# Performance work log

Measured on AMD Instinct MI355X. Metric: run time of the kernel, lower is better.

The kernel has to match this reference:

```python
import jax, jax.numpy as jnp
import numpy as np

B, P, D_IN = 128, 4096, 4   # frames, points/frame, xyz+time
NG = 16                      # number of trajectory groups
H1, H2, H3 = 64, 128, 512    # PointNet shared-MLP widths


def _init_mlp(key, dims):
    ks = jax.random.split(key, len(dims) - 1)
    params = []
    for k, (di, do) in zip(ks, zip(dims[:-1], dims[1:])):
        W = jax.random.normal(k, (di, do), dtype=jnp.float32) * (1.0 / np.sqrt(di))
        b = jnp.zeros((do,), dtype=jnp.float32)
        params.append((W, b))
    return params


def setup_inputs() -> dict:
    key = jax.random.key(0)
    k_pc, k_t, k_idx, k_g, k_l = jax.random.split(key, 5)
    pc = jax.random.normal(k_pc, (B, 3, P), dtype=jnp.float32)
    traj_time_batch = jax.random.uniform(k_t, (B, 1), dtype=jnp.float32)
    traj_inbatch_index = jnp.sort(jax.random.randint(k_idx, (B,), 0, NG)).astype(jnp.int32)
    (Wg1, bg1), (Wg2, bg2), (Wg3, bg3) = _init_mlp(k_g, [D_IN, H1, H2, H3])
    (Wl1, bl1), (Wl2, bl2), (Wl3, bl3) = _init_mlp(k_l, [D_IN, H1, H2, H3])
    return dict(pc=pc, traj_time_batch=traj_time_batch, traj_inbatch_index=traj_inbatch_index,
                Wg1=Wg1, bg1=bg1, Wg2=Wg2, bg2=bg2, Wg3=Wg3, bg3=bg3,
                Wl1=Wl1, bl1=bl1, Wl2=Wl2, bl2=bl2, Wl3=Wl3, bl3=bl3)


def _mlp(x, layers):
    # pointwise shared MLP: x [..., P, d_in] -> [..., P, d_out]
    for W, b in layers:
        x = jax.nn.relu(x @ W + b)
    return x


def reference(pc, traj_time_batch, traj_inbatch_index,
              Wg1, bg1, Wg2, bg2, Wg3, bg3,
              Wl1, bl1, Wl2, bl2, Wl3, bl3):
    b, _, p = pc.shape
    # append time channel: [B,3,P] + [B,1,P] -> [B,4,P]
    t = jnp.broadcast_to(traj_time_batch[..., None], (b, 1, p))
    feat = jnp.concatenate([pc, t], axis=1)
    x = jnp.swapaxes(feat, 1, 2)  # [B,P,4] points-last layout for pointwise MLP

    # global branch: shared MLP on every point, then max over all points of each trajectory group
    hg = _mlp(x, [(Wg1, bg1), (Wg2, bg2), (Wg3, bg3)])           # [B,P,H3]
    seg = jnp.repeat(traj_inbatch_index, p)                       # [B*P]
    gmax = jax.ops.segment_max(hg.reshape(b * p, -1), seg, num_segments=NG)  # [NG,H3]
    global_feat = gmax[traj_inbatch_index]                        # [B,H3] broadcast back per frame

    # local branch: per-frame PointNet encode (shared MLP + max over points)
    hl = _mlp(x, [(Wl1, bl1), (Wl2, bl2), (Wl3, bl3)])            # [B,P,H3]
    local_feat = hl.max(axis=1)                                   # [B,H3]

    z = jnp.concatenate([global_feat, local_feat], axis=1)        # [B,2*H3]
    input_features_vis = pc                                       # original pc (last dim == 4096, no slice)
    return (z, input_features_vis)
```

## Files before the change

kernel.cpp:

```cpp
#include <hip/hip_runtime.h>
#include <hip/hip_bf16.h>

#define NB   128
#define NP   4096
#define NGRP 16
#define C3   512

typedef __bf16 bf16x8 __attribute__((ext_vector_type(8)));
typedef __bf16 bf16x4 __attribute__((ext_vector_type(4)));
typedef float  f32x4  __attribute__((ext_vector_type(4)));

#define WS_W1F_G 0
#define WS_W1F_L 4096
#define WS_W2F_G 8192
#define WS_W2F_L 24576
#define WS_W3F_G 40960
#define WS_W3F_L 172032
#define WS_GMAX  303104

__global__ __launch_bounds__(256) void prep_kernel(
    const float* __restrict__ Wg1, const float* __restrict__ Wg2, const float* __restrict__ Wg3,
    const float* __restrict__ Wl1, const float* __restrict__ Wl2, const float* __restrict__ Wl3,
    char* __restrict__ ws) {
    const int t = blockIdx.x, tid = threadIdx.x;
    if (t == 36) {
        float* gmax = (float*)(ws + WS_GMAX);
        #pragma unroll
        for (int k = 0; k < 32; ++k) gmax[k * 256 + tid] = 0.0f;
        int c = tid >> 6, lane = tid & 63;
        int ch = c * 16 + (lane & 15);
        int kb = (lane >> 4) * 8;
        bf16x8 pg, pl;
        #pragma unroll
        for (int j = 0; j < 8; ++j) {
            int k = kb + j;
            pg[j] = (k < 4) ? (__bf16)Wg1[k * 64 + ch] : (__bf16)0.0f;
            pl[j] = (k < 4) ? (__bf16)Wl1[k * 64 + ch] : (__bf16)0.0f;
        }
        *(bf16x8*)((__bf16*)(ws + WS_W1F_G) + c * 512 + lane * 8) = pg;
        *(bf16x8*)((__bf16*)(ws + WS_W1F_L) + c * 512 + lane * 8) = pl;
        return;
    }
    __shared__ float tile[64][65];
    const float* src; __bf16* dst; int cBase, mMul, srcStride;
    if (t < 32) {
        int branch = t >> 4, rem = t & 15;
        int tk = rem >> 3, tc = rem & 7;
        src = (branch ? Wl3 : Wg3) + (size_t)(tk * 64) * 512 + tc * 64;
        dst = (__bf16*)(ws + (branch ? WS_W3F_L : WS_W3F_G));
        cBase = tc * 16 + tk * 2; mMul = 4; srcStride = 512;
    } else {
        int u = t - 32; int branch = u >> 1, tc = u & 1;
        src = (branch ? Wl2 : Wg2) + tc * 64;
        dst = (__bf16*)(ws + (branch ? WS_W2F_L : WS_W2F_G));
        cBase = tc * 8; mMul = 2; srcStride = 128;
    }
    {
        int r0 = tid >> 6, cl = tid & 63;
        #pragma unroll
        for (int p = 0; p < 16; ++p)
            tile[p * 4 + r0][cl] = src[(size_t)(p * 4 + r0) * srcStride + cl];
    }
    __syncthreads();
    int lane = tid & 63, l15 = lane & 15, q = lane >> 4;
    #pragma unroll
    for (int cc = 0; cc < 2; ++cc) {
        int pair = (tid >> 6) * 2 + cc;
        int mi = pair >> 1, ks = pair & 1;
        bf16x8 pk;
        #pragma unroll
        for (int j = 0; j < 8; ++j) pk[j] = (__bf16)tile[ks * 32 + q * 8 + j][mi * 16 + l15];
        *(bf16x8*)(dst + (cBase + mi * mMul + ks) * 512 + lane * 8) = pk;
    }
}

__global__ __launch_bounds__(512, 2) void main_kernel(
    const float* __restrict__ pc, const float* __restrict__ tt, const int* __restrict__ idx,
    const float* __restrict__ bg1, const float* __restrict__ bg2, const float* __restrict__ bg3,
    const float* __restrict__ bl1, const float* __restrict__ bl2, const float* __restrict__ bl3,
    float* __restrict__ out, char* __restrict__ ws) {
    __shared__ __align__(16) char smem[82688];
    __bf16* h2f = (__bf16*)smem;
    __bf16* h1f = (__bf16*)(smem + 65536);
    float*  b1s = (float*)(smem + 81920);
    float*  b2s = (float*)(smem + 82176);

    const int tid = threadIdx.x, lane = tid & 63, wave = tid >> 6;
    const int quad = lane >> 4, l15 = lane & 15;
    const int branch = blockIdx.y, frame = blockIdx.x;
    const int half = wave >> 2;
    const int slice = wave & 3;

    if (branch == 0) {
        const f32x4* ps = (const f32x4*)(pc + (size_t)frame * 3 * NP);
        f32x4* pd = (f32x4*)(out + NB * 2 * C3 + (size_t)frame * 3 * NP);
        #pragma unroll
        for (int j = 0; j < 6; ++j) pd[j * 512 + tid] = ps[j * 512 + tid];
    }

    const __bf16* w1g = (const __bf16*)(ws + (branch ? WS_W1F_L : WS_W1F_G));
    const __bf16* w2g = (const __bf16*)(ws + (branch ? WS_W2F_L : WS_W2F_G));
    const __bf16* w3g = (const __bf16*)(ws + (branch ? WS_W3F_L : WS_W3F_G));
    const float* b1 = branch ? bl1 : bg1;
    const float* b2 = branch ? bl2 : bg2;
    const float* b3 = branch ? bl3 : bg3;

    if (tid < 64)  b1s[tid] = b1[tid];
    if (tid < 128) b2s[tid] = b2[tid];

    bf16x8 a1[4];
    #pragma unroll
    for (int mi = 0; mi < 4; ++mi) a1[mi] = *(const bf16x8*)(w1g + mi * 512 + lane * 8);
    bf16x8 a2[2][2];
    #pragma unroll
    for (int mi = 0; mi < 2; ++mi)
        #pragma unroll
        for (int ks = 0; ks < 2; ++ks)
            a2[mi][ks] = *(const bf16x8*)(w2g + ((slice * 2 + mi) * 2 + ks) * 512 + lane * 8);
    bf16x8 aw[8][4];
    #pragma unroll
    for (int mi = 0; mi < 8; ++mi)
        #pragma unroll
        for (int ks = 0; ks < 4; ++ks)
            aw[mi][ks] = *(const bf16x8*)(w3g + ((slice * 8 + mi) * 4 + ks) * 512 + lane * 8);

    const float tval = tt[frame];
    const f32x4 zf = {0.0f, 0.0f, 0.0f, 0.0f};
    f32x4 runmax[8];
    #pragma unroll
    for (int mi = 0; mi < 8; ++mi) runmax[mi] = (f32x4){-1e30f, -1e30f, -1e30f, -1e30f};

    const float* pcx = pc + (size_t)frame * 3 * NP;
    const int pw = wave * 16 + l15;

    auto do_l1 = [&](float xx, float xy, float xz) {
        bf16x8 xb;
        #pragma unroll
        for (int j = 0; j < 8; ++j) xb[j] = (__bf16)0.0f;
        if (quad == 0) { xb[0] = (__bf16)xx; xb[1] = (__bf16)xy; xb[2] = (__bf16)xz; xb[3] = (__bf16)tval; }
        #pragma unroll
        for (int mi = 0; mi < 4; ++mi) {
            f32x4 c = __builtin_amdgcn_mfma_f32_16x16x32_bf16(a1[mi], xb, zf, 0, 0, 0);
            f32x4 bv = *(const f32x4*)(b1s + mi * 16 + quad * 4);
            bf16x4 pk;
            #pragma unroll
            for (int r = 0; r < 4; ++r) pk[r] = (__bf16)fmaxf(c[r] + bv[r], 0.0f);
            const int kq = (mi & 1) * 2 + (quad >> 1);
            *(bf16x4*)(h1f + (wave * 2 + (mi >> 1)) * 512 + kq * 128 + l15 * 8 + (quad & 1) * 4) = pk;
        }
    };
    auto do_l2 = [&](__bf16* hbn) {
        #pragma unroll
        for (int ni = 0; ni < 4; ++ni) {
            const int p16 = half * 4 + ni;
            bf16x8 q0 = *(const bf16x8*)(h1f + (p16 * 2 + 0) * 512 + lane * 8);
            bf16x8 q1 = *(const bf16x8*)(h1f + (p16 * 2 + 1) * 512 + lane * 8);
            #pragma unroll
            for (int mi = 0; mi < 2; ++mi) {
                f32x4 c = __builtin_amdgcn_mfma_f32_16x16x32_bf16(a2[mi][0], q0, zf, 0, 0, 0);
                c = __builtin_amdgcn_mfma_f32_16x16x32_bf16(a2[mi][1], q1, c, 0, 0, 0);
                f32x4 bv = *(const f32x4*)(b2s + slice * 32 + mi * 16 + quad * 4);
                bf16x4 pk;
                #pragma unroll
                for (int r = 0; r < 4; ++r) pk[r] = (__bf16)fmaxf(c[r] + bv[r], 0.0f);
                const int kq = mi * 2 + (quad >> 1);
                *(bf16x4*)(hbn + (p16 * 4 + slice) * 512 + kq * 128 + l15 * 8 + (quad & 1) * 4) = pk;
            }
        }
    };
    auto p2_pair = [&](const __bf16* hb, int p16base) {
        bf16x8 bhA[4], bhB[4];
        #pragma unroll
        for (int ks = 0; ks < 4; ++ks)
            bhA[ks] = *(const bf16x8*)(hb + (p16base * 4 + ks) * 512 + lane * 8);
        #pragma unroll
        for (int ks = 0; ks < 4; ++ks)
            bhB[ks] = *(const bf16x8*)(hb + ((p16base + 1) * 4 + ks) * 512 + lane * 8);
        #pragma unroll
        for (int u = 0; u < 2; ++u) {
            const bf16x8* cur = u ? bhB : bhA;
            #pragma unroll
            for (int mi = 0; mi < 8; ++mi) {
                f32x4 acc = __builtin_amdgcn_mfma_f32_16x16x32_bf16(aw[mi][0], cur[0], zf, 0, 0, 0);
                acc = __builtin_amdgcn_mfma_f32_16x16x32_bf16(aw[mi][1], cur[1], acc, 0, 0, 0);
                acc = __builtin_amdgcn_mfma_f32_16x16x32_bf16(aw[mi][2], cur[2], acc, 0, 0, 0);
                acc = __builtin_amdgcn_mfma_f32_16x16x32_bf16(aw[mi][3], cur[3], acc, 0, 0, 0);
                #pragma unroll
                for (int r = 0; r < 4; ++r) runmax[mi][r] = fmaxf(runmax[mi][r], acc[r]);
            }
        }
    };

    __syncthreads();

    {
        float xx = pcx[pw], xy = pcx[NP + pw], xz = pcx[2 * NP + pw];
        do_l1(xx, xy, xz);
        __syncthreads();
        do_l2(h2f);
    }

    for (int m = 0; m < 32; ++m) {
        __syncthreads();
        const __bf16* hb = h2f + (m & 1) * 16384;
        __bf16* hbn = h2f + ((m + 1) & 1) * 16384;
        const bool more = (m < 31);
        float nx = 0.f, ny = 0.f, nz = 0.f;
        if (more) {
            const int p = (m + 1) * 128 + pw;
            nx = pcx[p]; ny = pcx[NP + p]; nz = pcx[2 * NP + p];
        }
        p2_pair(hb, half * 4 + 0);
        if (more) do_l1(nx, ny, nz);
        __syncthreads();
        p2_pair(hb, half * 4 + 2);
        if (more) do_l2(hbn);
    }

    __syncthreads();
    float* fscr = (float*)h1f;
    #pragma unroll
    for (int mi = 0; mi < 8; ++mi) {
        f32x4 v = runmax[mi];
        #pragma unroll
        for (int d = 1; d < 16; d <<= 1) {
            #pragma unroll
            for (int r = 0; r < 4; ++r) v[r] = fmaxf(v[r], __shfl_xor(v[r], d));
        }
        if (l15 == 0) {
            #pragma unroll
            for (int r = 0; r < 4; ++r)
                fscr[half * 512 + slice * 128 + mi * 16 + quad * 4 + r] = v[r];
        }
    }
    __syncthreads();
    {
        const int g = idx[frame];
        float* gmax = (float*)(ws + WS_GMAX);
        float v = fmaxf(fscr[tid], fscr[512 + tid]);
        v = fmaxf(v + b3[tid], 0.0f);
        if (branch == 0)
            atomicMax((unsigned*)(gmax + g * C3 + tid), __float_as_uint(v));
        else
            out[(size_t)frame * (2 * C3) + C3 + tid] = v;
    }
}

__global__ void gather_kernel(const int* __restrict__ idx, const char* __restrict__ ws,
                              float* __restrict__ out) {
    int i = blockIdx.x * blockDim.x + threadIdx.x;
    int b = i >> 9, ch = i & 511;
    const float* gmax = (const float*)(ws + WS_GMAX);
    out[b * (2 * C3) + ch] = gmax[idx[b] * C3 + ch];
}

extern "C" void kernel_launch(void* const* d_in, const int* in_sizes, int n_in,
                              void* d_out, int out_size, void* d_ws, size_t ws_size,
                              hipStream_t stream) {
    const float* pc  = (const float*)d_in[0];
    const float* tt  = (const float*)d_in[1];
    const int*   idx = (const int*)d_in[2];
    const float* Wg1 = (const float*)d_in[3];  const float* bg1 = (const float*)d_in[4];
    const float* Wg2 = (const float*)d_in[5];  const float* bg2 = (const float*)d_in[6];
    const float* Wg3 = (const float*)d_in[7];  const float* bg3 = (const float*)d_in[8];
    const float* Wl1 = (const float*)d_in[9];  const float* bl1 = (const float*)d_in[10];
    const float* Wl2 = (const float*)d_in[11]; const float* bl2 = (const float*)d_in[12];
    const float* Wl3 = (const float*)d_in[13]; const float* bl3 = (const float*)d_in[14];
    float* out = (float*)d_out;
    char*  ws  = (char*)d_ws;

    prep_kernel<<<37, 256, 0, stream>>>(Wg1, Wg2, Wg3, Wl1, Wl2, Wl3, ws);
    main_kernel<<<dim3(128, 2), 512, 0, stream>>>(pc, tt, idx, bg1, bg2, bg3,
                                                  bl1, bl2, bl3, out, ws);
    gather_kernel<<<256, 256, 0, stream>>>(idx, ws, out);
}
```

Baseline: 242.8 us.

## Split each frame's points across four blocks and merge maxima with atomics

Each frame's 4096 points are now spread over four blocks of 1024 points, so the main kernel launches 1024 blocks instead of 256. Per-block shared memory and registers are halved, and the launch bound now requests four blocks per CU. Partial maxima are merged with atomicMax directly into the output and the group workspace, so the prep kernel zeroes the local-feature outputs first. This is meant to improve occupancy and load balance on a GPU with many CUs. The cost is more atomics and reloading the per-wave weight fragments in four times as many blocks.

```diff
diff --git a/kernel.cpp b/kernel.cpp
--- a/kernel.cpp
+++ b/kernel.cpp
@@ -21,8 +21,13 @@
 __global__ __launch_bounds__(256) void prep_kernel(
     const float* __restrict__ Wg1, const float* __restrict__ Wg2, const float* __restrict__ Wg3,
     const float* __restrict__ Wl1, const float* __restrict__ Wl2, const float* __restrict__ Wl3,
-    char* __restrict__ ws) {
+    float* __restrict__ out, char* __restrict__ ws) {
     const int t = blockIdx.x, tid = threadIdx.x;
+    if (t >= 37) {
+        #pragma unroll
+        for (int j = 0; j < 8; ++j) out[(t - 37) * 2048 + j * 256 + tid] = 0.0f;
+        return;
+    }
     if (t == 36) {
         float* gmax = (float*)(ws + WS_GMAX);
         #pragma unroll
@@ -74,28 +79,31 @@
     }
 }
 
-__global__ __launch_bounds__(512, 2) void main_kernel(
+__global__ __launch_bounds__(512, 4) void main_kernel(
     const float* __restrict__ pc, const float* __restrict__ tt, const int* __restrict__ idx,
     const float* __restrict__ bg1, const float* __restrict__ bg2, const float* __restrict__ bg3,
     const float* __restrict__ bl1, const float* __restrict__ bl2, const float* __restrict__ bl3,
     float* __restrict__ out, char* __restrict__ ws) {
-    __shared__ __align__(16) char smem[82688];
+    __shared__ __align__(16) char smem[41728];
     __bf16* h2f = (__bf16*)smem;
-    __bf16* h1f = (__bf16*)(smem + 65536);
-    float*  b1s = (float*)(smem + 81920);
-    float*  b2s = (float*)(smem + 82176);
+    __bf16* h1f = (__bf16*)(smem + 32768);
+    float*  b1s = (float*)(smem + 40960);
+    float*  b2s = (float*)(smem + 41216);
 
     const int tid = threadIdx.x, lane = tid & 63, wave = tid >> 6;
     const int quad = lane >> 4, l15 = lane & 15;
-    const int branch = blockIdx.y, frame = blockIdx.x;
-    const int half = wave >> 2;
-    const int slice = wave & 3;
+    const int branch = blockIdx.y;
+    const int frame = blockIdx.x >> 2, p0 = (blockIdx.x & 3) * 1024;
+
+    const float* pcx = pc + (size_t)frame * 3 * NP;
 
     if (branch == 0) {
-        const f32x4* ps = (const f32x4*)(pc + (size_t)frame * 3 * NP);
-        f32x4* pd = (f32x4*)(out + NB * 2 * C3 + (size_t)frame * 3 * NP);
-        #pragma unroll
-        for (int j = 0; j < 6; ++j) pd[j * 512 + tid] = ps[j * 512 + tid];
+        f32x4* pd = (f32x4*)(out + NB * 2 * C3 + (size_t)frame * 3 * NP + p0);
+        const f32x4* ps = (const f32x4*)(pcx + p0);
+        for (int i = tid; i < 768; i += 512) {
+            int r = i >> 8, col = i & 255;
+            pd[r * (NP / 4) + col] = ps[r * (NP / 4) + col];
+        }
     }
 
     const __bf16* w1g = (const __bf16*)(ws + (branch ? WS_W1F_L : WS_W1F_G));
@@ -111,27 +119,27 @@
     bf16x8 a1[4];
     #pragma unroll
     for (int mi = 0; mi < 4; ++mi) a1[mi] = *(const bf16x8*)(w1g + mi * 512 + lane * 8);
-    bf16x8 a2[2][2];
-    #pragma unroll
-    for (int mi = 0; mi < 2; ++mi)
-        #pragma unroll
-        for (int ks = 0; ks < 2; ++ks)
-            a2[mi][ks] = *(const bf16x8*)(w2g + ((slice * 2 + mi) * 2 + ks) * 512 + lane * 8);
-    bf16x8 aw[8][4];
-    #pragma unroll
-    for (int mi = 0; mi < 8; ++mi)
+    bf16x8 a2[2];
+    #pragma unroll
+    for (int ks = 0; ks < 2; ++ks)
+        a2[ks] = *(const bf16x8*)(w2g + (wave * 2 + ks) * 512 + lane * 8);
+    bf16x8 aw[4][4];
+    #pragma unroll
+    for (int mi = 0; mi < 4; ++mi)
         #pragma unroll
         for (int ks = 0; ks < 4; ++ks)
-            aw[mi][ks] = *(const bf16x8*)(w3g + ((slice * 8 + mi) * 4 + ks) * 512 + lane * 8);
+            aw[mi][ks] = *(const bf16x8*)(w3g + ((wave * 4 + mi) * 4 + ks) * 512 + lane * 8);
 
     const float tval = tt[frame];
     const f32x4 zf = {0.0f, 0.0f, 0.0f, 0.0f};
-    f32x4 runmax[8];
-    #pragma unroll
-    for (int mi = 0; mi < 8; ++mi) runmax[mi] = (f32x4){-1e30f, -1e30f, -1e30f, -1e30f};
-
-    const float* pcx = pc + (size_t)frame * 3 * NP;
-    const int pw = wave * 16 + l15;
+    f32x4 runmax[4];
+    #pragma unroll
+    for (int mi = 0; mi < 4; ++mi) runmax[mi] = (f32x4){-1e30f, -1e30f, -1e30f, -1e30f};
+
+    const bool l1wave = (wave < 4);
+    const int pw = (wave & 3) * 16 + l15;
+    const int kq2 = (wave * 2 + (quad >> 1)) & 3;
+    const int s2  = wave >> 1;
 
     auto do_l1 = [&](float xx, float xy, float xz) {
         bf16x8 xb;
@@ -146,103 +154,95 @@
             #pragma unroll
             for (int r = 0; r < 4; ++r) pk[r] = (__bf16)fmaxf(c[r] + bv[r], 0.0f);
             const int kq = (mi & 1) * 2 + (quad >> 1);
-            *(bf16x4*)(h1f + (wave * 2 + (mi >> 1)) * 512 + kq * 128 + l15 * 8 + (quad & 1) * 4) = pk;
+            *(bf16x4*)(h1f + ((wave & 3) * 2 + (mi >> 1)) * 512 + kq * 128 + l15 * 8 + (quad & 1) * 4) = pk;
         }
     };
     auto do_l2 = [&](__bf16* hbn) {
         #pragma unroll
         for (int ni = 0; ni < 4; ++ni) {
-            const int p16 = half * 4 + ni;
-            bf16x8 q0 = *(const bf16x8*)(h1f + (p16 * 2 + 0) * 512 + lane * 8);
-            bf16x8 q1 = *(const bf16x8*)(h1f + (p16 * 2 + 1) * 512 + lane * 8);
-            #pragma unroll
-            for (int mi = 0; mi < 2; ++mi) {
-                f32x4 c = __builtin_amdgcn_mfma_f32_16x16x32_bf16(a2[mi][0], q0, zf, 0, 0, 0);
-                c = __builtin_amdgcn_mfma_f32_16x16x32_bf16(a2[mi][1], q1, c, 0, 0, 0);
-                f32x4 bv = *(const f32x4*)(b2s + slice * 32 + mi * 16 + quad * 4);
-                bf16x4 pk;
-                #pragma unroll
-                for (int r = 0; r < 4; ++r) pk[r] = (__bf16)fmaxf(c[r] + bv[r], 0.0f);
-                const int kq = mi * 2 + (quad >> 1);
-                *(bf16x4*)(hbn + (p16 * 4 + slice) * 512 + kq * 128 + l15 * 8 + (quad & 1) * 4) = pk;
-            }
+            bf16x8 q0 = *(const bf16x8*)(h1f + (ni * 2 + 0) * 512 + lane * 8);
+            bf16x8 q1 = *(const bf16x8*)(h1f + (ni * 2 + 1) * 512 + lane * 8);
+            f32x4 c = __builtin_amdgcn_mfma_f32_16x16x32_bf16(a2[0], q0, zf, 0, 0, 0);
+            c = __builtin_amdgcn_mfma_f32_16x16x32_bf16(a2[1], q1, c, 0, 0, 0);
+            f32x4 bv = *(const f32x4*)(b2s + wave * 16 + quad * 4);
+            bf16x4 pk;
+            #pragma unroll
+            for (int r = 0; r < 4; ++r) pk[r] = (__bf16)fmaxf(c[r] + bv[r], 0.0f);
+            *(bf16x4*)(hbn + (ni * 4 + s2) * 512 + kq2 * 128 + l15 * 8 + (quad & 1) * 4) = pk;
         }
     };
-    auto p2_pair = [&](const __bf16* hb, int p16base) {
+    auto p2_pair = [&](const __bf16* hb, int nibase) {
         bf16x8 bhA[4], bhB[4];
         #pragma unroll
         for (int ks = 0; ks < 4; ++ks)
-            bhA[ks] = *(const bf16x8*)(hb + (p16base * 4 + ks) * 512 + lane * 8);
+            bhA[ks] = *(const bf16x8*)(hb + (nibase * 4 + ks) * 512 + lane * 8);
         #pragma unroll
         for (int ks = 0; ks < 4; ++ks)
-            bhB[ks] = *(const bf16x8*)(hb + ((p16base + 1) * 4 + ks) * 512 + lane * 8);
+            bhB[ks] = *(const bf16x8*)(hb + ((nibase + 1) * 4 + ks) * 512 + lane * 8);
         #pragma unroll
         for (int u = 0; u < 2; ++u) {
             const bf16x8* cur = u ? bhB : bhA;
-            #pragma unroll
-            for (int mi = 0; mi < 8; ++mi) {
-                f32x4 acc = __builtin_amdgcn_mfma_f32_16x16x32_bf16(aw[mi][0], cur[0], zf, 0, 0, 0);
-                acc = __builtin_amdgcn_mfma_f32_16x16x32_bf16(aw[mi][1], cur[1], acc, 0, 0, 0);
-                acc = __builtin_amdgcn_mfma_f32_16x16x32_bf16(aw[mi][2], cur[2], acc, 0, 0, 0);
-                acc = __builtin_amdgcn_mfma_f32_16x16x32_bf16(aw[mi][3], cur[3], acc, 0, 0, 0);
+            f32x4 acc[4];
+            #pragma unroll
+            for (int ks = 0; ks < 4; ++ks)
                 #pragma unroll
-                for (int r = 0; r < 4; ++r) runmax[mi][r] = fmaxf(runmax[mi][r], acc[r]);
+                for (int mi = 0; mi < 4; ++mi)
+                    acc[mi] = __builtin_amdgcn_mfma_f32_16x16x32_bf16(
+                        aw[mi][ks], cur[ks], ks ? acc[mi] : zf, 0, 0, 0);
+            #pragma unroll
+            for (int mi = 0; mi < 4; ++mi)
+                #pragma unroll
+                for (int r = 0; r < 4; ++r)
+                    runmax[mi][r] = fmaxf(runmax[mi][r], acc[mi][r]);
+        }
+    };
+
+    __syncthreads();
+
+    if (l1wave) {
+        float xx = pcx[p0 + pw], xy = pcx[NP + p0 + pw], xz = pcx[2 * NP + p0 + pw];
+        do_l1(xx, xy, xz);
+    }
+    __syncthreads();
+    do_l2(h2f);
+
+    for (int m = 0; m < 16; ++m) {
+        __syncthreads();
+        const __bf16* hb = h2f + (m & 1) * 8192;
+        __bf16* hbn = h2f + ((m + 1) & 1) * 8192;
+        const bool more = (m < 15);
+        float nx = 0.f, ny = 0.f, nz = 0.f;
+        if (more && l1wave) {
+            const int p = p0 + (m + 1) * 64 + pw;
+            nx = pcx[p]; ny = pcx[NP + p]; nz = pcx[2 * NP + p];
+        }
+        p2_pair(hb, 0);
+        if (more && l1wave) do_l1(nx, ny, nz);
+        __syncthreads();
+        p2_pair(hb, 2);
+        if (more) do_l2(hbn);
+    }
+
+    const int g = idx[frame];
+    float* gmax = (float*)(ws + WS_GMAX);
+    unsigned* dst = (branch == 0) ? (unsigned*)(gmax + g * C3)
+                                  : (unsigned*)(out + (size_t)frame * (2 * C3) + C3);
+    #pragma unroll
+    for (int mi = 0; mi < 4; ++mi) {
+        f32x4 v = runmax[mi];
+        #pragma unroll
+        for (int d = 1; d < 16; d <<= 1) {
+            #pragma unroll
+            for (int r = 0; r < 4; ++r) v[r] = fmaxf(v[r], __shfl_xor(v[r], d));
+        }
+        if (l15 == 0) {
+            #pragma unroll
+            for (int r = 0; r < 4; ++r) {
+                const int ch = wave * 64 + mi * 16 + quad * 4 + r;
+                const float fv = fmaxf(v[r] + b3[ch], 0.0f);
+                atomicMax(dst + ch, __float_as_uint(fv));
             }
         }
-    };
-
-    __syncthreads();
-
-    {
-        float xx = pcx[pw], xy = pcx[NP + pw], xz = pcx[2 * NP + pw];
-        do_l1(xx, xy, xz);
-        __syncthreads();
-        do_l2(h2f);
-    }
-
-    for (int m = 0; m < 32; ++m) {
-        __syncthreads();
-        const __bf16* hb = h2f + (m & 1) * 16384;
-        __bf16* hbn = h2f + ((m + 1) & 1) * 16384;
-        const bool more = (m < 31);
-        float nx = 0.f, ny = 0.f, nz = 0.f;
-        if (more) {
-            const int p = (m + 1) * 128 + pw;
-            nx = pcx[p]; ny = pcx[NP + p]; nz = pcx[2 * NP + p];
-        }
-        p2_pair(hb, half * 4 + 0);
-        if (more) do_l1(nx, ny, nz);
-        __syncthreads();
-        p2_pair(hb, half * 4 + 2);
-        if (more) do_l2(hbn);
-    }
-
-    __syncthreads();
-    float* fscr = (float*)h1f;
-    #pragma unroll
-    for (int mi = 0; mi < 8; ++mi) {
-        f32x4 v = runmax[mi];
-        #pragma unroll
-        for (int d = 1; d < 16; d <<= 1) {
-            #pragma unroll
-            for (int r = 0; r < 4; ++r) v[r] = fmaxf(v[r], __shfl_xor(v[r], d));
-        }
-        if (l15 == 0) {
-            #pragma unroll
-            for (int r = 0; r < 4; ++r)
-                fscr[half * 512 + slice * 128 + mi * 16 + quad * 4 + r] = v[r];
-        }
-    }
-    __syncthreads();
-    {
-        const int g = idx[frame];
-        float* gmax = (float*)(ws + WS_GMAX);
-        float v = fmaxf(fscr[tid], fscr[512 + tid]);
-        v = fmaxf(v + b3[tid], 0.0f);
-        if (branch == 0)
-            atomicMax((unsigned*)(gmax + g * C3 + tid), __float_as_uint(v));
-        else
-            out[(size_t)frame * (2 * C3) + C3 + tid] = v;
     }
 }
 
@@ -269,8 +269,8 @@
     float* out = (float*)d_out;
     char*  ws  = (char*)d_ws;
 
-    prep_kernel<<<37, 256, 0, stream>>>(Wg1, Wg2, Wg3, Wl1, Wl2, Wl3, ws);
-    main_kernel<<<dim3(128, 2), 512, 0, stream>>>(pc, tt, idx, bg1, bg2, bg3,
+    prep_kernel<<<101, 256, 0, stream>>>(Wg1, Wg2, Wg3, Wl1, Wl2, Wl3, out, ws);
+    main_kernel<<<dim3(512, 2), 512, 0, stream>>>(pc, tt, idx, bg1, bg2, bg3,
                                                   bl1, bl2, bl3, out, ws);
     gather_kernel<<<256, 256, 0, stream>>>(idx, ws, out);
 }
```

Result: slower. 736.2 us (+203.2%).
